# Optimization experiments

Measured on AMD Instinct MI355X. Metric: run time of the kernel, lower is better.

Reference implementation:

```python
import jax, jax.numpy as jnp
import numpy as np

B, T, D_IN, H, D_OUT = 64, 512, 512, 1024, 512

def _uniform(key, shape, bound):
    return jax.random.uniform(key, shape, jnp.float32, -bound, bound)

def setup_inputs() -> dict:
    key = jax.random.key(0)
    ks = jax.random.split(key, 12)
    bnd = 1.0 / np.sqrt(H)  # PyTorch nn.RNN / nn.Linear init bound
    return {
        "x": jax.random.normal(ks[0], (B, T, D_IN), jnp.float32),
        "W_ih0": _uniform(ks[1], (H, D_IN), bnd),
        "W_hh0": _uniform(ks[2], (H, H), bnd),
        "b_ih0": _uniform(ks[3], (H,), bnd),
        "b_hh0": _uniform(ks[4], (H,), bnd),
        "W_ih1": _uniform(ks[5], (H, H), bnd),
        "W_hh1": _uniform(ks[6], (H, H), bnd),
        "b_ih1": _uniform(ks[7], (H,), bnd),
        "b_hh1": _uniform(ks[8], (H,), bnd),
        "W_fc": _uniform(ks[9], (D_OUT, H), bnd),
        "b_fc": _uniform(ks[10], (D_OUT,), bnd),
    }

def _rnn_layer(seq, W_ih, W_hh, b_ih, b_hh):
    # seq: [B, T, D]; tanh vanilla RNN, h0 = 0 (as in the torch forward)
    pre = jnp.einsum('btd,hd->bth', seq, W_ih) + b_ih  # input GEMM batched over time
    h0 = jnp.zeros((seq.shape[0], W_hh.shape[0]), seq.dtype)
    def step(h, p):
        h = jnp.tanh(p + h @ W_hh.T + b_hh)
        return h, h
    _, hs = jax.lax.scan(step, h0, jnp.swapaxes(pre, 0, 1))  # [T, B, H]
    return jnp.swapaxes(hs, 0, 1)  # [B, T, H]

def reference(x, W_ih0, W_hh0, b_ih0, b_hh0, W_ih1, W_hh1, b_ih1, b_hh1, W_fc, b_fc):
    h1 = _rnn_layer(x, W_ih0, W_hh0, b_ih0, b_hh0)
    h2 = _rnn_layer(h1, W_ih1, W_hh1, b_ih1, b_hh1)
    last = h2[:, -1, :]  # only the final timestep feeds the head
    return last @ W_fc.T + b_fc
```

## Files before the change

kernel.cpp:

```cpp
#include <hip/hip_runtime.h>
#include <stdint.h>

#define BB   64
#define TT   512
#define DIN  512
#define HH   1024
#define DOUT 512

#define GROUPS        4
#define ROWS          16
#define WGS_PER_GROUP 16
#define NSLICE        64
#define THREADS       512
#define NW            8
#define PSTR          18
#define SENT          0x7fff7fffu

typedef __attribute__((ext_vector_type(8))) short frag8;
typedef __attribute__((ext_vector_type(4))) float f32x4;
typedef __attribute__((ext_vector_type(4))) unsigned int u32x4;

union U4F8 { u32x4 u; frag8 f; };

__device__ __forceinline__ float bf2f(unsigned short u) {
  union { unsigned int i; float f; } v; v.i = ((unsigned int)u) << 16; return v.f;
}
__device__ __forceinline__ unsigned short f2bf(float f) {
  union { float f; unsigned int i; } v; v.f = f;
  unsigned int x = v.i;
  x += 0x7fffu + ((x >> 16) & 1u);
  return (unsigned short)(x >> 16);
}
__device__ __forceinline__ frag8 ld8f32(const float* p) {
  frag8 r;
#pragma unroll
  for (int j = 0; j < 8; ++j) r[j] = (short)f2bf(p[j]);
  return r;
}

__device__ __forceinline__ bool ldx4_poll(frag8 a[4], const unsigned short* p) {
  u32x4 t0, t1, t2, t3;
  asm volatile(
      "global_load_dwordx4 %0, %4, off sc1\n\t"
      "global_load_dwordx4 %1, %4, off offset:64 sc1\n\t"
      "global_load_dwordx4 %2, %4, off offset:128 sc1\n\t"
      "global_load_dwordx4 %3, %4, off offset:192 sc1\n\t"
      "s_waitcnt vmcnt(0)"
      : "=&v"(t0), "=&v"(t1), "=&v"(t2), "=&v"(t3)
      : "v"(p)
      : "memory");
  bool ok = (t0[0] != SENT) & (t0[1] != SENT) & (t0[2] != SENT) & (t0[3] != SENT)
          & (t1[0] != SENT) & (t1[1] != SENT) & (t1[2] != SENT) & (t1[3] != SENT)
          & (t2[0] != SENT) & (t2[1] != SENT) & (t2[2] != SENT) & (t2[3] != SENT)
          & (t3[0] != SENT) & (t3[1] != SENT) & (t3[2] != SENT) & (t3[3] != SENT);
  U4F8 u;
  u.u = t0; a[0] = u.f;  u.u = t1; a[1] = u.f;
  u.u = t2; a[2] = u.f;  u.u = t3; a[3] = u.f;
  return __ballot(ok) == ~0ull;
}
__device__ __forceinline__ bool ldx8_poll(frag8 a[4], frag8 b[4],
                                          const unsigned short* pa,
                                          const unsigned short* pb) {
  u32x4 t0, t1, t2, t3, s0, s1, s2, s3;
  asm volatile(
      "global_load_dwordx4 %0, %8, off sc1\n\t"
      "global_load_dwordx4 %1, %8, off offset:64 sc1\n\t"
      "global_load_dwordx4 %2, %8, off offset:128 sc1\n\t"
      "global_load_dwordx4 %3, %8, off offset:192 sc1\n\t"
      "global_load_dwordx4 %4, %9, off sc1\n\t"
      "global_load_dwordx4 %5, %9, off offset:64 sc1\n\t"
      "global_load_dwordx4 %6, %9, off offset:128 sc1\n\t"
      "global_load_dwordx4 %7, %9, off offset:192 sc1\n\t"
      "s_waitcnt vmcnt(0)"
      : "=&v"(t0), "=&v"(t1), "=&v"(t2), "=&v"(t3),
        "=&v"(s0), "=&v"(s1), "=&v"(s2), "=&v"(s3)
      : "v"(pa), "v"(pb)
      : "memory");
  bool ok = (t0[0] != SENT) & (t0[1] != SENT) & (t0[2] != SENT) & (t0[3] != SENT)
          & (t1[0] != SENT) & (t1[1] != SENT) & (t1[2] != SENT) & (t1[3] != SENT)
          & (t2[0] != SENT) & (t2[1] != SENT) & (t2[2] != SENT) & (t2[3] != SENT)
          & (t3[0] != SENT) & (t3[1] != SENT) & (t3[2] != SENT) & (t3[3] != SENT)
          & (s0[0] != SENT) & (s0[1] != SENT) & (s0[2] != SENT) & (s0[3] != SENT)
          & (s1[0] != SENT) & (s1[1] != SENT) & (s1[2] != SENT) & (s1[3] != SENT)
          & (s2[0] != SENT) & (s2[1] != SENT) & (s2[2] != SENT) & (s2[3] != SENT)
          & (s3[0] != SENT) & (s3[1] != SENT) & (s3[2] != SENT) & (s3[3] != SENT);
  U4F8 u;
  u.u = t0; a[0] = u.f;  u.u = t1; a[1] = u.f;
  u.u = t2; a[2] = u.f;  u.u = t3; a[3] = u.f;
  u.u = s0; b[0] = u.f;  u.u = s1; b[1] = u.f;
  u.u = s2; b[2] = u.f;  u.u = s3; b[3] = u.f;
  return __ballot(ok) == ~0ull;
}
__device__ __forceinline__ void st32_sc1(unsigned int* p, unsigned int v) {
  asm volatile("global_store_dword %0, %1, off sc1" :: "v"(p), "v"(v) : "memory");
}

template<int KIN, bool L0>
__device__ void scan_body(const void* Xv,
                          const float* Wih, const float* Whh,
                          const float* bih, const float* bhh,
                          unsigned short* S,
                          int g, int s, float* parts)
{
  constexpr int KIT_IN = KIN / (NW * 32);
  constexpr int KIT_HH = HH  / (NW * 32);

  const int j0  = s * NSLICE;
  const int r0  = g * ROWS;
  const int tid = threadIdx.x;
  const int w   = tid >> 6;
  const int l   = tid & 63;
  const int lm  = l & 15;
  const int lq  = l >> 4;

  frag8 wih_f[KIT_IN][4];
  frag8 whh_f[KIT_HH][4];
#pragma unroll
  for (int kit = 0; kit < KIT_IN; ++kit)
#pragma unroll
    for (int nt = 0; nt < 4; ++nt) {
      int n = j0 + nt * 16 + lm;
      int k = w * (KIN / NW) + kit * 32 + lq * 8;
      wih_f[kit][nt] = ld8f32(Wih + (size_t)n * KIN + k);
    }
#pragma unroll
  for (int kit = 0; kit < KIT_HH; ++kit)
#pragma unroll
    for (int nt = 0; nt < 4; ++nt) {
      int n = j0 + nt * 16 + lm;
      int k = w * (HH / NW) + kit * 32 + lq * 8;
      whh_f[kit][nt] = ld8f32(Whh + (size_t)n * HH + k);
    }

  const int erow = tid & 15;
  const int ecg  = tid >> 4;
  float bias2[2];
#pragma unroll
  for (int j = 0; j < 2; ++j) {
    int c = j0 + ecg * 2 + j;
    bias2[j] = bih[c] + bhh[c];
  }

  for (int t = 0; t < TT; ++t) {
    f32x4 acc[4];
#pragma unroll
    for (int nt = 0; nt < 4; ++nt) acc[nt] = (f32x4){0.f, 0.f, 0.f, 0.f};

    if constexpr (L0) {
      const float* xr = (const float*)Xv
          + ((size_t)(r0 + lm) * TT + t) * KIN + w * (KIN / NW) + lq * 8;
#pragma unroll
      for (int kit = 0; kit < KIT_IN; ++kit) {
        float4 x0 = *(const float4*)(xr + kit * 32);
        float4 x1 = *(const float4*)(xr + kit * 32 + 4);
        frag8 a;
        a[0] = (short)f2bf(x0.x); a[1] = (short)f2bf(x0.y);
        a[2] = (short)f2bf(x0.z); a[3] = (short)f2bf(x0.w);
        a[4] = (short)f2bf(x1.x); a[5] = (short)f2bf(x1.y);
        a[6] = (short)f2bf(x1.z); a[7] = (short)f2bf(x1.w);
#pragma unroll
        for (int nt = 0; nt < 4; ++nt)
          acc[nt] = __builtin_amdgcn_mfma_f32_16x16x32_bf16(a, wih_f[kit][nt], acc[nt], 0, 0, 0);
      }
      if (t > 0) {
        const unsigned short* ph = S + ((size_t)(r0 + lm) * TT + (t - 1)) * HH
                                     + w * (HH / NW) + lq * 8;
        frag8 hf[KIT_HH];
        while (!ldx4_poll(hf, ph)) {}
#pragma unroll
        for (int kit = 0; kit < KIT_HH; ++kit)
#pragma unroll
          for (int nt = 0; nt < 4; ++nt)
            acc[nt] = __builtin_amdgcn_mfma_f32_16x16x32_bf16(hf[kit], whh_f[kit][nt], acc[nt], 0, 0, 0);
      }
    } else {
      const unsigned short* px = (const unsigned short*)Xv
          + ((size_t)(r0 + lm) * TT + t) * KIN + w * (KIN / NW) + lq * 8;
      if (t > 0) {
        const unsigned short* ph = S + ((size_t)(r0 + lm) * TT + (t - 1)) * HH
                                     + w * (HH / NW) + lq * 8;
        frag8 xf[KIT_IN], hf[KIT_HH];
        while (!ldx8_poll(xf, hf, px, ph)) {}
#pragma unroll
        for (int kit = 0; kit < KIT_IN; ++kit)
#pragma unroll
          for (int nt = 0; nt < 4; ++nt)
            acc[nt] = __builtin_amdgcn_mfma_f32_16x16x32_bf16(xf[kit], wih_f[kit][nt], acc[nt], 0, 0, 0);
#pragma unroll
        for (int kit = 0; kit < KIT_HH; ++kit)
#pragma unroll
          for (int nt = 0; nt < 4; ++nt)
            acc[nt] = __builtin_amdgcn_mfma_f32_16x16x32_bf16(hf[kit], whh_f[kit][nt], acc[nt], 0, 0, 0);
      } else {
        frag8 xf[KIT_IN];
        while (!ldx4_poll(xf, px)) {}
#pragma unroll
        for (int kit = 0; kit < KIT_IN; ++kit)
#pragma unroll
          for (int nt = 0; nt < 4; ++nt)
            acc[nt] = __builtin_amdgcn_mfma_f32_16x16x32_bf16(xf[kit], wih_f[kit][nt], acc[nt], 0, 0, 0);
      }
    }

#pragma unroll
    for (int nt = 0; nt < 4; ++nt)
#pragma unroll
      for (int r = 0; r < 4; ++r)
        parts[((w * 4 + nt) * 16 + lq * 4 + r) * PSTR + lm] = acc[nt][r];
    __syncthreads();

    unsigned int hb2 = 0;
#pragma unroll
    for (int j = 0; j < 2; ++j) {
      int c  = ecg * 2 + j;
      int nt = c >> 4;
      int lc = c & 15;
      float sm = 0.f;
#pragma unroll
      for (int w8 = 0; w8 < NW; ++w8)
        sm += parts[((w8 * 4 + nt) * 16 + erow) * PSTR + lc];
      float u = sm + bias2[j];
      float e = __expf(2.0f * u);
      float hv = 1.0f - 2.0f / (e + 1.0f);
      hb2 |= (unsigned int)f2bf(hv) << (16 * j);
    }
    unsigned short* dst = S + ((size_t)(r0 + erow) * TT + t) * HH + j0 + ecg * 2;
    st32_sc1((unsigned int*)dst, hb2);
    __syncthreads();
  }
}

__global__ __launch_bounds__(THREADS, 1)
void rnn_fused(const float* x,
               const float* Wih0, const float* Whh0, const float* bih0, const float* bhh0,
               const float* Wih1, const float* Whh1, const float* bih1, const float* bhh1,
               unsigned short* h1seq, unsigned short* h2seq)
{
  __shared__ float parts[NW * 4 * 16 * PSTR];
  const int wg = blockIdx.x;
  if (wg < GROUPS * WGS_PER_GROUP) {
    const int g = wg / WGS_PER_GROUP, s = wg % WGS_PER_GROUP;
    scan_body<DIN, true>(x, Wih0, Whh0, bih0, bhh0, h1seq, g, s, parts);
  } else {
    const int wg2 = wg - GROUPS * WGS_PER_GROUP;
    const int g = wg2 / WGS_PER_GROUP, s = wg2 % WGS_PER_GROUP;
    scan_body<HH, false>(h1seq, Wih1, Whh1, bih1, bhh1, h2seq, g, s, parts);
  }
}

__global__ void poison_kernel(uint4* __restrict__ p, int n4) {
  int i  = blockIdx.x * blockDim.x + threadIdx.x;
  int st = gridDim.x * blockDim.x;
  const uint4 v = make_uint4(SENT, SENT, SENT, SENT);
  for (; i < n4; i += st) p[i] = v;
}

__global__ void fc_kernel(const unsigned short* __restrict__ h2seq,
                          const float* __restrict__ Wfc,
                          const float* __restrict__ bfc,
                          float* __restrict__ out)
{
  int idx = blockIdx.x * blockDim.x + threadIdx.x;
  int m = idx >> 9;
  int n = idx & 511;
  const unsigned short* hp = h2seq + ((size_t)m * TT + (TT - 1)) * HH;
  const float*          wp = Wfc + (size_t)n * HH;
  float acc = 0.f;
#pragma unroll 4
  for (int k = 0; k < HH; k += 4) {
    ushort4 hv = *(const ushort4*)(hp + k);
    float4  wv = *(const float4*)(wp + k);
    acc += bf2f(hv.x) * wv.x + bf2f(hv.y) * wv.y
         + bf2f(hv.z) * wv.z + bf2f(hv.w) * wv.w;
  }
  out[idx] = acc + bfc[n];
}

extern "C" void kernel_launch(void* const* d_in, const int* in_sizes, int n_in,
                              void* d_out, int out_size, void* d_ws, size_t ws_size,
                              hipStream_t stream)
{
  const float* x    = (const float*)d_in[0];
  const float* Wih0 = (const float*)d_in[1];
  const float* Whh0 = (const float*)d_in[2];
  const float* bih0 = (const float*)d_in[3];
  const float* bhh0 = (const float*)d_in[4];
  const float* Wih1 = (const float*)d_in[5];
  const float* Whh1 = (const float*)d_in[6];
  const float* bih1 = (const float*)d_in[7];
  const float* bhh1 = (const float*)d_in[8];
  const float* Wfc  = (const float*)d_in[9];
  const float* bfc  = (const float*)d_in[10];

  unsigned char* ws = (unsigned char*)d_ws;
  unsigned short* h1seq = (unsigned short*)ws;
  unsigned short* h2seq = (unsigned short*)(ws + (size_t)BB * TT * HH * 2);

  poison_kernel<<<4096, 256, 0, stream>>>(
      (uint4*)ws, (int)(((size_t)BB * TT * HH * 2 * 2) / 16));

  rnn_fused<<<2 * GROUPS * WGS_PER_GROUP, THREADS, 0, stream>>>(
      x, Wih0, Whh0, bih0, bhh0, Wih1, Whh1, bih1, bhh1, h1seq, h2seq);

  fc_kernel<<<(BB * DOUT) / 256, 256, 0, stream>>>(h2seq, Wfc, bfc, (float*)d_out);
}
```

Before: 2.104 ms.

## Prefetch next-step inputs and double-buffer partial sums to drop a barrier

The input-projection operand for step t+1 is now loaded ahead of time: layer 0 prefetches the fp32 x rows into registers after the h poll, and layer 1 polls the next h1 row right after storing its output. The input MFMAs can then run before waiting on the recurrent state. The LDS partial-sum buffer is double-buffered by step parity, which lets the trailing __syncthreads be removed. This aims to take input load latency and one barrier off the serial recurrence path, at the cost of more registers and LDS and a subtler ordering argument for buffer reuse.

```diff
diff --git a/kernel.cpp b/kernel.cpp
--- a/kernel.cpp
+++ b/kernel.cpp
@@ -14,6 +14,7 @@
 #define THREADS       512
 #define NW            8
 #define PSTR          18
+#define PBUF          (NW * 4 * 16 * PSTR)
 #define SENT          0x7fff7fffu
 
 typedef __attribute__((ext_vector_type(8))) short frag8;
@@ -58,39 +59,6 @@
   u.u = t2; a[2] = u.f;  u.u = t3; a[3] = u.f;
   return __ballot(ok) == ~0ull;
 }
-__device__ __forceinline__ bool ldx8_poll(frag8 a[4], frag8 b[4],
-                                          const unsigned short* pa,
-                                          const unsigned short* pb) {
-  u32x4 t0, t1, t2, t3, s0, s1, s2, s3;
-  asm volatile(
-      "global_load_dwordx4 %0, %8, off sc1\n\t"
-      "global_load_dwordx4 %1, %8, off offset:64 sc1\n\t"
-      "global_load_dwordx4 %2, %8, off offset:128 sc1\n\t"
-      "global_load_dwordx4 %3, %8, off offset:192 sc1\n\t"
-      "global_load_dwordx4 %4, %9, off sc1\n\t"
-      "global_load_dwordx4 %5, %9, off offset:64 sc1\n\t"
-      "global_load_dwordx4 %6, %9, off offset:128 sc1\n\t"
-      "global_load_dwordx4 %7, %9, off offset:192 sc1\n\t"
-      "s_waitcnt vmcnt(0)"
-      : "=&v"(t0), "=&v"(t1), "=&v"(t2), "=&v"(t3),
-        "=&v"(s0), "=&v"(s1), "=&v"(s2), "=&v"(s3)
-      : "v"(pa), "v"(pb)
-      : "memory");
-  bool ok = (t0[0] != SENT) & (t0[1] != SENT) & (t0[2] != SENT) & (t0[3] != SENT)
-          & (t1[0] != SENT) & (t1[1] != SENT) & (t1[2] != SENT) & (t1[3] != SENT)
-          & (t2[0] != SENT) & (t2[1] != SENT) & (t2[2] != SENT) & (t2[3] != SENT)
-          & (t3[0] != SENT) & (t3[1] != SENT) & (t3[2] != SENT) & (t3[3] != SENT)
-          & (s0[0] != SENT) & (s0[1] != SENT) & (s0[2] != SENT) & (s0[3] != SENT)
-          & (s1[0] != SENT) & (s1[1] != SENT) & (s1[2] != SENT) & (s1[3] != SENT)
-          & (s2[0] != SENT) & (s2[1] != SENT) & (s2[2] != SENT) & (s2[3] != SENT)
-          & (s3[0] != SENT) & (s3[1] != SENT) & (s3[2] != SENT) & (s3[3] != SENT);
-  U4F8 u;
-  u.u = t0; a[0] = u.f;  u.u = t1; a[1] = u.f;
-  u.u = t2; a[2] = u.f;  u.u = t3; a[3] = u.f;
-  u.u = s0; b[0] = u.f;  u.u = s1; b[1] = u.f;
-  u.u = s2; b[2] = u.f;  u.u = s3; b[3] = u.f;
-  return __ballot(ok) == ~0ull;
-}
 __device__ __forceinline__ void st32_sc1(unsigned int* p, unsigned int v) {
   asm volatile("global_store_dword %0, %1, off sc1" :: "v"(p), "v"(v) : "memory");
 }
@@ -141,72 +109,87 @@
     bias2[j] = bih[c] + bhh[c];
   }
 
+  const size_t koff = (size_t)w * (KIN / NW) + (size_t)lq * 8;
+
+  float4 xa[2 * KIT_IN];
+  frag8  xf[KIT_IN];
+  if constexpr (L0) {
+    const float* xr = (const float*)Xv + ((size_t)(r0 + lm) * TT + 0) * KIN + koff;
+#pragma unroll
+    for (int kit = 0; kit < KIT_IN; ++kit) {
+      xa[2 * kit]     = *(const float4*)(xr + kit * 32);
+      xa[2 * kit + 1] = *(const float4*)(xr + kit * 32 + 4);
+    }
+  } else {
+    const unsigned short* px = (const unsigned short*)Xv
+        + ((size_t)(r0 + lm) * TT + 0) * KIN + koff;
+    while (!ldx4_poll(xf, px)) {}
+  }
+
   for (int t = 0; t < TT; ++t) {
     f32x4 acc[4];
 #pragma unroll
     for (int nt = 0; nt < 4; ++nt) acc[nt] = (f32x4){0.f, 0.f, 0.f, 0.f};
 
     if constexpr (L0) {
-      const float* xr = (const float*)Xv
-          + ((size_t)(r0 + lm) * TT + t) * KIN + w * (KIN / NW) + lq * 8;
 #pragma unroll
       for (int kit = 0; kit < KIT_IN; ++kit) {
-        float4 x0 = *(const float4*)(xr + kit * 32);
-        float4 x1 = *(const float4*)(xr + kit * 32 + 4);
+        const float* f0 = (const float*)&xa[2 * kit];
+        const float* f1 = (const float*)&xa[2 * kit + 1];
         frag8 a;
-        a[0] = (short)f2bf(x0.x); a[1] = (short)f2bf(x0.y);
-        a[2] = (short)f2bf(x0.z); a[3] = (short)f2bf(x0.w);
-        a[4] = (short)f2bf(x1.x); a[5] = (short)f2bf(x1.y);
-        a[6] = (short)f2bf(x1.z); a[7] = (short)f2bf(x1.w);
+#pragma unroll
+        for (int j = 0; j < 4; ++j) {
+          a[j]     = (short)f2bf(f0[j]);
+          a[4 + j] = (short)f2bf(f1[j]);
+        }
 #pragma unroll
         for (int nt = 0; nt < 4; ++nt)
           acc[nt] = __builtin_amdgcn_mfma_f32_16x16x32_bf16(a, wih_f[kit][nt], acc[nt], 0, 0, 0);
       }
-      if (t > 0) {
-        const unsigned short* ph = S + ((size_t)(r0 + lm) * TT + (t - 1)) * HH
-                                     + w * (HH / NW) + lq * 8;
-        frag8 hf[KIT_HH];
-        while (!ldx4_poll(hf, ph)) {}
-#pragma unroll
-        for (int kit = 0; kit < KIT_HH; ++kit)
-#pragma unroll
-          for (int nt = 0; nt < 4; ++nt)
-            acc[nt] = __builtin_amdgcn_mfma_f32_16x16x32_bf16(hf[kit], whh_f[kit][nt], acc[nt], 0, 0, 0);
-      }
     } else {
-      const unsigned short* px = (const unsigned short*)Xv
-          + ((size_t)(r0 + lm) * TT + t) * KIN + w * (KIN / NW) + lq * 8;
-      if (t > 0) {
-        const unsigned short* ph = S + ((size_t)(r0 + lm) * TT + (t - 1)) * HH
-                                     + w * (HH / NW) + lq * 8;
-        frag8 xf[KIT_IN], hf[KIT_HH];
-        while (!ldx8_poll(xf, hf, px, ph)) {}
-#pragma unroll
-        for (int kit = 0; kit < KIT_IN; ++kit)
-#pragma unroll
-          for (int nt = 0; nt < 4; ++nt)
-            acc[nt] = __builtin_amdgcn_mfma_f32_16x16x32_bf16(xf[kit], wih_f[kit][nt], acc[nt], 0, 0, 0);
-#pragma unroll
-        for (int kit = 0; kit < KIT_HH; ++kit)
-#pragma unroll
-          for (int nt = 0; nt < 4; ++nt)
-            acc[nt] = __builtin_amdgcn_mfma_f32_16x16x32_bf16(hf[kit], whh_f[kit][nt], acc[nt], 0, 0, 0);
-      } else {
-        frag8 xf[KIT_IN];
-        while (!ldx4_poll(xf, px)) {}
-#pragma unroll
-        for (int kit = 0; kit < KIT_IN; ++kit)
-#pragma unroll
-          for (int nt = 0; nt < 4; ++nt)
-            acc[nt] = __builtin_amdgcn_mfma_f32_16x16x32_bf16(xf[kit], wih_f[kit][nt], acc[nt], 0, 0, 0);
-      }
-    }
-
+#pragma unroll
+      for (int kit = 0; kit < KIT_IN; ++kit)
+#pragma unroll
+        for (int nt = 0; nt < 4; ++nt)
+          acc[nt] = __builtin_amdgcn_mfma_f32_16x16x32_bf16(xf[kit], wih_f[kit][nt], acc[nt], 0, 0, 0);
+    }
+
+    if (t > 0) {
+      const unsigned short* ph = S + ((size_t)(r0 + lm) * TT + (t - 1)) * HH
+                                   + (size_t)w * (HH / NW) + lq * 8;
+      frag8 hf[KIT_HH];
+      while (!ldx4_poll(hf, ph)) {}
+      if constexpr (L0) {
+        if (t + 1 < TT) {
+          const float* xr = (const float*)Xv
+              + ((size_t)(r0 + lm) * TT + (t + 1)) * KIN + koff;
+#pragma unroll
+          for (int kit = 0; kit < KIT_IN; ++kit) {
+            xa[2 * kit]     = *(const float4*)(xr + kit * 32);
+            xa[2 * kit + 1] = *(const float4*)(xr + kit * 32 + 4);
+          }
+        }
+      }
+#pragma unroll
+      for (int kit = 0; kit < KIT_HH; ++kit)
+#pragma unroll
+        for (int nt = 0; nt < 4; ++nt)
+          acc[nt] = __builtin_amdgcn_mfma_f32_16x16x32_bf16(hf[kit], whh_f[kit][nt], acc[nt], 0, 0, 0);
+    } else if constexpr (L0) {
+      const float* xr = (const float*)Xv + ((size_t)(r0 + lm) * TT + 1) * KIN + koff;
+#pragma unroll
+      for (int kit = 0; kit < KIT_IN; ++kit) {
+        xa[2 * kit]     = *(const float4*)(xr + kit * 32);
+        xa[2 * kit + 1] = *(const float4*)(xr + kit * 32 + 4);
+      }
+    }
+
+    float* pb = parts + (t & 1) * PBUF;
 #pragma unroll
     for (int nt = 0; nt < 4; ++nt)
 #pragma unroll
       for (int r = 0; r < 4; ++r)
-        parts[((w * 4 + nt) * 16 + lq * 4 + r) * PSTR + lm] = acc[nt][r];
+        pb[((w * 4 + nt) * 16 + lq * 4 + r) * PSTR + lm] = acc[nt][r];
     __syncthreads();
 
     unsigned int hb2 = 0;
@@ -218,7 +201,7 @@
       float sm = 0.f;
 #pragma unroll
       for (int w8 = 0; w8 < NW; ++w8)
-        sm += parts[((w8 * 4 + nt) * 16 + erow) * PSTR + lc];
+        sm += pb[((w8 * 4 + nt) * 16 + erow) * PSTR + lc];
       float u = sm + bias2[j];
       float e = __expf(2.0f * u);
       float hv = 1.0f - 2.0f / (e + 1.0f);
@@ -226,7 +209,14 @@
     }
     unsigned short* dst = S + ((size_t)(r0 + erow) * TT + t) * HH + j0 + ecg * 2;
     st32_sc1((unsigned int*)dst, hb2);
-    __syncthreads();
+
+    if constexpr (!L0) {
+      if (t + 1 < TT) {
+        const unsigned short* px = (const unsigned short*)Xv
+            + ((size_t)(r0 + lm) * TT + (t + 1)) * KIN + koff;
+        while (!ldx4_poll(xf, px)) {}
+      }
+    }
   }
 }
 
@@ -236,7 +226,7 @@
                const float* Wih1, const float* Whh1, const float* bih1, const float* bhh1,
                unsigned short* h1seq, unsigned short* h2seq)
 {
-  __shared__ float parts[NW * 4 * 16 * PSTR];
+  __shared__ float parts[2 * PBUF];
   const int wg = blockIdx.x;
   if (wg < GROUPS * WGS_PER_GROUP) {
     const int g = wg / WGS_PER_GROUP, s = wg % WGS_PER_GROUP;
```

Measured after the change: 1.960 ms. -6.8%, faster.
